# Kernel optimization log

Measured on AMD Instinct MI355X. Metric: run time of the kernel, lower is better.

The kernel has to match this reference:

```python
import jax, jax.numpy as jnp
import numpy as np

T = 16384
IN = 14
H = 100
OUT = 1


def setup_inputs() -> dict:
    key = jax.random.key(0)
    ks = jax.random.split(key, 11)
    s_in = 1.0 / np.sqrt(H)
    x = jax.random.normal(ks[0], (T, IN), dtype=jnp.float32)
    # PyTorch nn.GRU params: weight_ih_l{k} [3H, in], weight_hh_l{k} [3H, H], biases [3H]; gate order (r, z, n)
    w_ih0 = jax.random.uniform(ks[1], (3 * H, IN), minval=-s_in, maxval=s_in, dtype=jnp.float32)
    w_hh0 = jax.random.uniform(ks[2], (3 * H, H), minval=-s_in, maxval=s_in, dtype=jnp.float32)
    b_ih0 = jax.random.uniform(ks[3], (3 * H,), minval=-s_in, maxval=s_in, dtype=jnp.float32)
    b_hh0 = jax.random.uniform(ks[4], (3 * H,), minval=-s_in, maxval=s_in, dtype=jnp.float32)
    w_ih1 = jax.random.uniform(ks[5], (3 * H, H), minval=-s_in, maxval=s_in, dtype=jnp.float32)
    w_hh1 = jax.random.uniform(ks[6], (3 * H, H), minval=-s_in, maxval=s_in, dtype=jnp.float32)
    b_ih1 = jax.random.uniform(ks[7], (3 * H,), minval=-s_in, maxval=s_in, dtype=jnp.float32)
    b_hh1 = jax.random.uniform(ks[8], (3 * H,), minval=-s_in, maxval=s_in, dtype=jnp.float32)
    fc_w = jax.random.uniform(ks[9], (OUT, H), minval=-s_in, maxval=s_in, dtype=jnp.float32)
    fc_b = jax.random.uniform(ks[10], (OUT,), minval=-s_in, maxval=s_in, dtype=jnp.float32)
    return {"x": x, "w_ih0": w_ih0, "w_hh0": w_hh0, "b_ih0": b_ih0, "b_hh0": b_hh0,
            "w_ih1": w_ih1, "w_hh1": w_hh1, "b_ih1": b_ih1, "b_hh1": b_hh1,
            "fc_w": fc_w, "fc_b": fc_b}


def _gru_layer(x_seq, w_ih, w_hh, b_ih, b_hh):
    # x_seq: [T, D_in] (batch=1 squeezed). Precompute input projections for all steps.
    gi = x_seq @ w_ih.T + b_ih  # [T, 3H]

    def step(h, gi_t):
        gh = h @ w_hh.T + b_hh  # [3H]
        i_r, i_z, i_n = jnp.split(gi_t, 3)
        h_r, h_z, h_n = jnp.split(gh, 3)
        r = jax.nn.sigmoid(i_r + h_r)
        z = jax.nn.sigmoid(i_z + h_z)
        n = jnp.tanh(i_n + r * h_n)
        h_new = (1.0 - z) * n + z * h
        return h_new, h_new

    h0 = jnp.zeros((w_hh.shape[1],), dtype=x_seq.dtype)
    _, out = jax.lax.scan(step, h0, gi)
    return out  # [T, H]


def reference(x, w_ih0, w_hh0, b_ih0, b_hh0, w_ih1, w_hh1, b_ih1, b_hh1, fc_w, fc_b):
    h1 = _gru_layer(x, w_ih0, w_hh0, b_ih0, b_hh0)   # layer 0: [T, H]
    h2 = _gru_layer(h1, w_ih1, w_hh1, b_ih1, b_hh1)  # layer 1: [T, H]
    out = h2 @ fc_w.T + fc_b                          # [T, 1]
    return out[-1]                                     # [1]
```

## Files before the change

### kernel.cpp

```cpp
#include <hip/hip_runtime.h>
#include <math.h>

#define T_STEPS 16384
#define IN_DIM  14
#define H_DIM   100
#define G_DIM   300

typedef float f2 __attribute__((ext_vector_type(2)));

#define REP25(M) M(0) M(1) M(2) M(3) M(4) M(5) M(6) M(7) M(8) M(9) M(10) M(11) \
                 M(12) M(13) M(14) M(15) M(16) M(17) M(18) M(19) M(20) M(21) M(22) M(23) M(24)

__global__ void gi0_kernel(const float* __restrict__ x,
                           const float* __restrict__ w_ih0,
                           const float* __restrict__ b_ih0,
                           float* __restrict__ gi0) {
    int e = blockIdx.x * blockDim.x + threadIdx.x;
    if (e >= T_STEPS * G_DIM) return;
    int t = e / G_DIM;
    int j = e - t * G_DIM;
    const float* xr = x + t * IN_DIM;
    const float* wr = w_ih0 + j * IN_DIM;
    float acc = b_ih0[j];
    #pragma unroll
    for (int k = 0; k < IN_DIM; ++k) acc = fmaf(xr[k], wr[k], acc);
    gi0[e] = acc;
}

__global__ __launch_bounds__(512, 2)
void gru_seq_kernel(const float* __restrict__ gi0,
                    const float* __restrict__ w_hh0,
                    const float* __restrict__ b_hh0,
                    const float* __restrict__ w_ih1,
                    const float* __restrict__ b_ih1,
                    const float* __restrict__ w_hh1,
                    const float* __restrict__ b_hh1,
                    const float* __restrict__ fc_w,
                    const float* __restrict__ fc_b,
                    float* __restrict__ out) {
    __shared__ __align__(16) float hbuf[256];
    __shared__ __align__(16) float gh[3 * G_DIM];

    const int tid = threadIdx.x;
    const int idx = (tid < 450) ? tid : 449;
    const int g   = idx / 150;
    const int pr  = idx - g * 150;
    const int r0  = 2 * pr;
    const bool active = (tid < 450);

    const float* wbase; const float* bbase;
    if (g == 0)      { wbase = w_hh0; bbase = b_hh0; }
    else if (g == 1) { wbase = w_ih1; bbase = b_ih1; }
    else             { wbase = w_hh1; bbase = b_hh1; }
    const float bias0 = bbase[r0];
    const float bias1 = bbase[r0 + 1];
    const int hoff4 = (g == 2) ? 32 : 0;
    const int ghw   = (g * G_DIM) / 2 + pr;

    #define DECLK(k) f2 w0a_##k, w0b_##k, w1a_##k, w1b_##k;
    REP25(DECLK)
    #undef DECLK
    {
        const float4* p0 = reinterpret_cast<const float4*>(wbase + (size_t)r0 * H_DIM);
        const float4* p1 = reinterpret_cast<const float4*>(wbase + (size_t)(r0 + 1) * H_DIM);
        #define LOADK(k) { float4 A = p0[k]; w0a_##k.x = A.x; w0a_##k.y = A.y; w0b_##k.x = A.z; w0b_##k.y = A.w; \
                           float4 B = p1[k]; w1a_##k.x = B.x; w1a_##k.y = B.y; w1b_##k.x = B.z; w1b_##k.y = B.w; }
        REP25(LOADK)
        #undef LOADK
    }

    if (tid < 256) hbuf[tid] = 0.0f;
    __syncthreads();

    const float4* hb4 = reinterpret_cast<const float4*>(hbuf);
    float2* gh2 = reinterpret_cast<float2*>(gh);

    for (int i = 0; i <= T_STEPS; ++i) {
        float gr = 0.f, gz = 0.f, gn = 0.f;
        if (tid < H_DIM && i < T_STEPS) {
            const float* p = gi0 + (size_t)i * G_DIM + tid;
            gr = p[0]; gz = p[H_DIM]; gn = p[2 * H_DIM];
        }

        f2 acc0, acc1, acc2, acc3;
        acc0.x = bias0; acc0.y = 0.0f;
        acc1.x = 0.0f;  acc1.y = 0.0f;
        acc2.x = bias1; acc2.y = 0.0f;
        acc3.x = 0.0f;  acc3.y = 0.0f;
        #define DOTK(k) { float4 V = hb4[hoff4 + k]; \
                          f2 va, vb; va.x = V.x; va.y = V.y; vb.x = V.z; vb.y = V.w; \
                          acc0 += w0a_##k * va; acc1 += w0b_##k * vb; \
                          acc2 += w1a_##k * va; acc3 += w1b_##k * vb; }
        REP25(DOTK)
        #undef DOTK
        if (active) {
            float a = (acc0.x + acc1.x) + (acc0.y + acc1.y);
            float b = (acc2.x + acc3.x) + (acc2.y + acc3.y);
            gh2[ghw] = make_float2(a, b);
        }
        __syncthreads();

        if (tid < H_DIM) {
            if (i < T_STEPS) {
                float r = 1.0f / (1.0f + expf(-(gr + gh[tid])));
                float z = 1.0f / (1.0f + expf(-(gz + gh[H_DIM + tid])));
                float n = tanhf(gn + r * gh[2 * H_DIM + tid]);
                float hp = hbuf[tid];
                hbuf[tid] = (1.0f - z) * n + z * hp;
            }
        } else if (tid >= 256 && tid < 256 + H_DIM) {
            if (i >= 1) {
                int j = tid - 256;
                float r = 1.0f / (1.0f + expf(-(gh[G_DIM + j] + gh[2 * G_DIM + j])));
                float z = 1.0f / (1.0f + expf(-(gh[G_DIM + H_DIM + j] + gh[2 * G_DIM + H_DIM + j])));
                float n = tanhf(gh[G_DIM + 2 * H_DIM + j] + r * gh[2 * G_DIM + 2 * H_DIM + j]);
                float hp = hbuf[128 + j];
                hbuf[128 + j] = (1.0f - z) * n + z * hp;
            }
        }
        __syncthreads();
    }

    if (tid < 64) {
        float s = 0.0f;
        for (int j = tid; j < H_DIM; j += 64) s = fmaf(fc_w[j], hbuf[128 + j], s);
        #pragma unroll
        for (int off = 32; off > 0; off >>= 1) s += __shfl_down(s, off);
        if (tid == 0) out[0] = s + fc_b[0];
    }
}

extern "C" void kernel_launch(void* const* d_in, const int* in_sizes, int n_in,
                              void* d_out, int out_size, void* d_ws, size_t ws_size,
                              hipStream_t stream) {
    const float* x     = (const float*)d_in[0];
    const float* w_ih0 = (const float*)d_in[1];
    const float* w_hh0 = (const float*)d_in[2];
    const float* b_ih0 = (const float*)d_in[3];
    const float* b_hh0 = (const float*)d_in[4];
    const float* w_ih1 = (const float*)d_in[5];
    const float* w_hh1 = (const float*)d_in[6];
    const float* b_ih1 = (const float*)d_in[7];
    const float* b_hh1 = (const float*)d_in[8];
    const float* fc_w  = (const float*)d_in[9];
    const float* fc_b  = (const float*)d_in[10];
    float* out = (float*)d_out;
    float* gi0 = (float*)d_ws;

    const int total = T_STEPS * G_DIM;
    gi0_kernel<<<(total + 255) / 256, 256, 0, stream>>>(x, w_ih0, b_ih0, gi0);
    gru_seq_kernel<<<1, 512, 0, stream>>>(gi0, w_hh0, b_hh0, w_ih1, b_ih1,
                                          w_hh1, b_hh1, fc_w, fc_b, out);
}
```

Before: 15.66 ms.

## Broadcast hidden state via scalar loads from global ring, one row per thread

Each step now publishes the new hidden states of both layers to a 64-slot ring buffer in global workspace. Each wavefront reads the previous step's hidden vector with s_load_dwordx16 scalar loads after invalidating the scalar cache, so the values arrive in SGPRs and no longer come through per-lane LDS broadcast reads. The block grows to 960 threads (15 waves) so each thread holds one weight row (50 float2 registers) instead of two, which halves the per-thread FMA chain. The cost is two global scalar-load round trips plus global stores on the serial critical path of every step. Correctness also depends on the ring writes becoming visible to scalar loads across the barrier.

```diff
diff --git a/kernel.cpp b/kernel.cpp
--- a/kernel.cpp
+++ b/kernel.cpp
@@ -6,10 +6,12 @@
 #define H_DIM   100
 #define G_DIM   300
 
-typedef float f2 __attribute__((ext_vector_type(2)));
-
-#define REP25(M) M(0) M(1) M(2) M(3) M(4) M(5) M(6) M(7) M(8) M(9) M(10) M(11) \
-                 M(12) M(13) M(14) M(15) M(16) M(17) M(18) M(19) M(20) M(21) M(22) M(23) M(24)
+typedef float f2v  __attribute__((ext_vector_type(2)));
+typedef float f16v __attribute__((ext_vector_type(16)));
+
+#define RING_SLOTS 64
+#define SLOT_F     128
+#define GI0_OFS    16384
 
 __global__ void gi0_kernel(const float* __restrict__ x,
                            const float* __restrict__ w_ih0,
@@ -27,8 +29,12 @@
     gi0[e] = acc;
 }
 
-__global__ __launch_bounds__(512, 2)
+__global__ __attribute__((amdgpu_flat_work_group_size(960, 960), amdgpu_waves_per_eu(4)))
 void gru_seq_kernel(const float* __restrict__ gi0,
+                    const float* __restrict__ ring1,
+                    const float* __restrict__ ring2,
+                    float* __restrict__ ring1w,
+                    float* __restrict__ ring2w,
                     const float* __restrict__ w_hh0,
                     const float* __restrict__ b_hh0,
                     const float* __restrict__ w_ih1,
@@ -41,39 +47,52 @@
     __shared__ __align__(16) float hbuf[256];
     __shared__ __align__(16) float gh[3 * G_DIM];
 
-    const int tid = threadIdx.x;
-    const int idx = (tid < 450) ? tid : 449;
-    const int g   = idx / 150;
-    const int pr  = idx - g * 150;
-    const int r0  = 2 * pr;
-    const bool active = (tid < 450);
-
-    const float* wbase; const float* bbase;
-    if (g == 0)      { wbase = w_hh0; bbase = b_hh0; }
-    else if (g == 1) { wbase = w_ih1; bbase = b_ih1; }
-    else             { wbase = w_hh1; bbase = b_hh1; }
-    const float bias0 = bbase[r0];
-    const float bias1 = bbase[r0 + 1];
-    const int hoff4 = (g == 2) ? 32 : 0;
-    const int ghw   = (g * G_DIM) / 2 + pr;
-
-    #define DECLK(k) f2 w0a_##k, w0b_##k, w1a_##k, w1b_##k;
-    REP25(DECLK)
-    #undef DECLK
+    const int tid  = threadIdx.x;
+    const int lane = tid & 63;
+    const int wid  = tid >> 6;
+    const int gsel = wid / 5;
+    const int rig  = (wid - gsel * 5) * 64 + lane;
+    const bool active = rig < G_DIM;
+    const int row  = active ? rig : (G_DIM - 1);
+
+    const float* wmat; const float* bvec;
+    if (gsel == 0)      { wmat = w_hh0; bvec = b_hh0; }
+    else if (gsel == 1) { wmat = w_ih1; bvec = b_ih1; }
+    else                { wmat = w_hh1; bvec = b_hh1; }
+    const float bias = bvec[row];
+    const int ghidx = gsel * G_DIM + rig;
+
+    f2v w_0,w_1,w_2,w_3,w_4,w_5,w_6,w_7,w_8,w_9,w_10,w_11,w_12,w_13,w_14,w_15,w_16,w_17,
+        w_18,w_19,w_20,w_21,w_22,w_23,w_24,w_25,w_26,w_27,w_28,w_29,w_30,w_31,w_32,w_33,
+        w_34,w_35,w_36,w_37,w_38,w_39,w_40,w_41,w_42,w_43,w_44,w_45,w_46,w_47,w_48,w_49;
     {
-        const float4* p0 = reinterpret_cast<const float4*>(wbase + (size_t)r0 * H_DIM);
-        const float4* p1 = reinterpret_cast<const float4*>(wbase + (size_t)(r0 + 1) * H_DIM);
-        #define LOADK(k) { float4 A = p0[k]; w0a_##k.x = A.x; w0a_##k.y = A.y; w0b_##k.x = A.z; w0b_##k.y = A.w; \
-                           float4 B = p1[k]; w1a_##k.x = B.x; w1a_##k.y = B.y; w1b_##k.x = B.z; w1b_##k.y = B.w; }
-        REP25(LOADK)
-        #undef LOADK
-    }
+        const float4* wp = reinterpret_cast<const float4*>(wmat + (size_t)row * H_DIM);
+        #define LOADW(k, a, b) { float4 A = wp[k]; w_##a.x = A.x; w_##a.y = A.y; w_##b.x = A.z; w_##b.y = A.w; }
+        LOADW(0,0,1)   LOADW(1,2,3)   LOADW(2,4,5)   LOADW(3,6,7)   LOADW(4,8,9)
+        LOADW(5,10,11) LOADW(6,12,13) LOADW(7,14,15) LOADW(8,16,17) LOADW(9,18,19)
+        LOADW(10,20,21) LOADW(11,22,23) LOADW(12,24,25) LOADW(13,26,27) LOADW(14,28,29)
+        LOADW(15,30,31) LOADW(16,32,33) LOADW(17,34,35) LOADW(18,36,37) LOADW(19,38,39)
+        LOADW(20,40,41) LOADW(21,42,43) LOADW(22,44,45) LOADW(23,46,47) LOADW(24,48,49)
+        #undef LOADW
+    }
+    #define PIN(k) asm volatile("" : "+v"(w_##k));
+    PIN(0) PIN(1) PIN(2) PIN(3) PIN(4) PIN(5) PIN(6) PIN(7) PIN(8) PIN(9)
+    PIN(10) PIN(11) PIN(12) PIN(13) PIN(14) PIN(15) PIN(16) PIN(17) PIN(18) PIN(19)
+    PIN(20) PIN(21) PIN(22) PIN(23) PIN(24) PIN(25) PIN(26) PIN(27) PIN(28) PIN(29)
+    PIN(30) PIN(31) PIN(32) PIN(33) PIN(34) PIN(35) PIN(36) PIN(37) PIN(38) PIN(39)
+    PIN(40) PIN(41) PIN(42) PIN(43) PIN(44) PIN(45) PIN(46) PIN(47) PIN(48) PIN(49)
+    #undef PIN
 
     if (tid < 256) hbuf[tid] = 0.0f;
+    if (tid < 128) {
+        ring1w[63 * SLOT_F + tid] = 0.0f;
+        ring2w[63 * SLOT_F + tid] = 0.0f;
+        ring2w[tid] = 0.0f;
+    }
     __syncthreads();
 
-    const float4* hb4 = reinterpret_cast<const float4*>(hbuf);
-    float2* gh2 = reinterpret_cast<float2*>(gh);
+    const int gu = __builtin_amdgcn_readfirstlane(gsel);
+    const float* myring = (gu == 2) ? ring2 : ring1;
 
     for (int i = 0; i <= T_STEPS; ++i) {
         float gr = 0.f, gz = 0.f, gn = 0.f;
@@ -82,31 +101,66 @@
             gr = p[0]; gz = p[H_DIM]; gn = p[2 * H_DIM];
         }
 
-        f2 acc0, acc1, acc2, acc3;
-        acc0.x = bias0; acc0.y = 0.0f;
-        acc1.x = 0.0f;  acc1.y = 0.0f;
-        acc2.x = bias1; acc2.y = 0.0f;
-        acc3.x = 0.0f;  acc3.y = 0.0f;
-        #define DOTK(k) { float4 V = hb4[hoff4 + k]; \
-                          f2 va, vb; va.x = V.x; va.y = V.y; vb.x = V.z; vb.y = V.w; \
-                          acc0 += w0a_##k * va; acc1 += w0b_##k * vb; \
-                          acc2 += w1a_##k * va; acc3 += w1b_##k * vb; }
-        REP25(DOTK)
-        #undef DOTK
-        if (active) {
-            float a = (acc0.x + acc1.x) + (acc0.y + acc1.y);
-            float b = (acc2.x + acc3.x) + (acc2.y + acc3.y);
-            gh2[ghw] = make_float2(a, b);
-        }
+        const int slot = (i - 1) & (RING_SLOTS - 1);
+        const float* hptr = myring + (slot << 7);
+        __builtin_amdgcn_s_dcache_inv();
+        f16v ha, hb, hc; f2v hd;
+        asm volatile(
+            "s_load_dwordx16 %0, %4, 0x0\n\t"
+            "s_load_dwordx16 %1, %4, 0x40\n\t"
+            "s_load_dwordx16 %2, %4, 0x80\n\t"
+            "s_load_dwordx2  %3, %4, 0xc0\n\t"
+            "s_waitcnt lgkmcnt(0)"
+            : "=&s"(ha), "=&s"(hb), "=&s"(hc), "=&s"(hd)
+            : "s"(hptr)
+            : "memory");
+
+        f2v acc_a, acc_b;
+        acc_a.x = bias; acc_a.y = 0.0f;
+        acc_b.x = 0.0f; acc_b.y = 0.0f;
+        #define FMA(ACC, WK, HV, J) { f2v hp; hp.x = (HV)[2*(J)]; hp.y = (HV)[2*(J)+1]; ACC += WK * hp; }
+        FMA(acc_a, w_0, ha, 0) FMA(acc_a, w_1, ha, 1) FMA(acc_a, w_2, ha, 2) FMA(acc_a, w_3, ha, 3)
+        FMA(acc_a, w_4, ha, 4) FMA(acc_a, w_5, ha, 5) FMA(acc_a, w_6, ha, 6) FMA(acc_a, w_7, ha, 7)
+        FMA(acc_a, w_8, hb, 0) FMA(acc_a, w_9, hb, 1) FMA(acc_a, w_10, hb, 2) FMA(acc_a, w_11, hb, 3)
+        FMA(acc_a, w_12, hb, 4) FMA(acc_a, w_13, hb, 5) FMA(acc_a, w_14, hb, 6) FMA(acc_a, w_15, hb, 7)
+        FMA(acc_a, w_16, hc, 0) FMA(acc_a, w_17, hc, 1) FMA(acc_a, w_18, hc, 2) FMA(acc_a, w_19, hc, 3)
+        FMA(acc_a, w_20, hc, 4) FMA(acc_a, w_21, hc, 5) FMA(acc_a, w_22, hc, 6) FMA(acc_a, w_23, hc, 7)
+        FMA(acc_a, w_24, hd, 0)
+
+        const float* hptr2 = hptr + 50;
+        f16v ea, eb, ec; f2v ed;
+        asm volatile(
+            "s_load_dwordx16 %0, %4, 0x0\n\t"
+            "s_load_dwordx16 %1, %4, 0x40\n\t"
+            "s_load_dwordx16 %2, %4, 0x80\n\t"
+            "s_load_dwordx2  %3, %4, 0xc0\n\t"
+            "s_waitcnt lgkmcnt(0)"
+            : "=&s"(ea), "=&s"(eb), "=&s"(ec), "=&s"(ed)
+            : "s"(hptr2)
+            : "memory");
+
+        FMA(acc_b, w_25, ea, 0) FMA(acc_b, w_26, ea, 1) FMA(acc_b, w_27, ea, 2) FMA(acc_b, w_28, ea, 3)
+        FMA(acc_b, w_29, ea, 4) FMA(acc_b, w_30, ea, 5) FMA(acc_b, w_31, ea, 6) FMA(acc_b, w_32, ea, 7)
+        FMA(acc_b, w_33, eb, 0) FMA(acc_b, w_34, eb, 1) FMA(acc_b, w_35, eb, 2) FMA(acc_b, w_36, eb, 3)
+        FMA(acc_b, w_37, eb, 4) FMA(acc_b, w_38, eb, 5) FMA(acc_b, w_39, eb, 6) FMA(acc_b, w_40, eb, 7)
+        FMA(acc_b, w_41, ec, 0) FMA(acc_b, w_42, ec, 1) FMA(acc_b, w_43, ec, 2) FMA(acc_b, w_44, ec, 3)
+        FMA(acc_b, w_45, ec, 4) FMA(acc_b, w_46, ec, 5) FMA(acc_b, w_47, ec, 6) FMA(acc_b, w_48, ec, 7)
+        FMA(acc_b, w_49, ed, 0)
+        #undef FMA
+
+        if (active) gh[ghidx] = (acc_a.x + acc_a.y) + (acc_b.x + acc_b.y);
         __syncthreads();
 
+        const int wslot = i & (RING_SLOTS - 1);
         if (tid < H_DIM) {
             if (i < T_STEPS) {
                 float r = 1.0f / (1.0f + expf(-(gr + gh[tid])));
                 float z = 1.0f / (1.0f + expf(-(gz + gh[H_DIM + tid])));
                 float n = tanhf(gn + r * gh[2 * H_DIM + tid]);
                 float hp = hbuf[tid];
-                hbuf[tid] = (1.0f - z) * n + z * hp;
+                float hn = (1.0f - z) * n + z * hp;
+                hbuf[tid] = hn;
+                ring1w[wslot * SLOT_F + tid] = hn;
             }
         } else if (tid >= 256 && tid < 256 + H_DIM) {
             if (i >= 1) {
@@ -115,7 +169,9 @@
                 float z = 1.0f / (1.0f + expf(-(gh[G_DIM + H_DIM + j] + gh[2 * G_DIM + H_DIM + j])));
                 float n = tanhf(gh[G_DIM + 2 * H_DIM + j] + r * gh[2 * G_DIM + 2 * H_DIM + j]);
                 float hp = hbuf[128 + j];
-                hbuf[128 + j] = (1.0f - z) * n + z * hp;
+                float hn = (1.0f - z) * n + z * hp;
+                hbuf[128 + j] = hn;
+                ring2w[wslot * SLOT_F + j] = hn;
             }
         }
         __syncthreads();
@@ -145,10 +201,15 @@
     const float* fc_w  = (const float*)d_in[9];
     const float* fc_b  = (const float*)d_in[10];
     float* out = (float*)d_out;
-    float* gi0 = (float*)d_ws;
+
+    float* ws   = (float*)d_ws;
+    float* r1   = ws;
+    float* r2   = ws + 8192;
+    float* gi0  = ws + GI0_OFS;
 
     const int total = T_STEPS * G_DIM;
     gi0_kernel<<<(total + 255) / 256, 256, 0, stream>>>(x, w_ih0, b_ih0, gi0);
-    gru_seq_kernel<<<1, 512, 0, stream>>>(gi0, w_hh0, b_hh0, w_ih1, b_ih1,
+    gru_seq_kernel<<<1, 960, 0, stream>>>(gi0, r1, r2, r1, r2,
+                                          w_hh0, b_hh0, w_ih1, b_ih1,
                                           w_hh1, b_hh1, fc_w, fc_b, out);
 }
```

Result: slower. 23.83 ms (+52.2%).
